# Kernel tuning notes

Hardware: AMD Instinct MI355X
Metric: run time of the kernel (lower is better)

Reference implementation:

```python
import jax, jax.numpy as jnp
import numpy as np

B, F, H, LAT = 4, 64, 128, 512
N_CALLS = 16          # n_calls=2, module multiplies by 8
NEG = 0.2             # leaky-relu slope
EPS = 1e-5            # InstanceNorm2d eps

# hypernetwork output layout: w_in[F,3F], b_in[F], w_mid[F,F], b_mid[F], w_out[F,F], b_out[F], w_short[F,3F], b_short[F]
_sizes = [3*F*F, F, F*F, F, F*F, F, 3*F*F, F]
_off = np.cumsum([0] + _sizes)
HYP_OUT = int(_off[-1])


def _sobel_kernel():
    # SinSobel: smoothing (cos) x derivative (sin) separable 5x5 gradient filters
    lin = np.linspace(-1.0, 1.0, 5)
    d = np.sin(lin * np.pi / 2.0)
    s = np.cos(lin * np.pi / 2.0)
    gx = np.outer(s, d)                      # d/dx
    gy = np.outer(d, s)                      # d/dy
    k = np.stack([gx, gy])[:, None]          # [2,1,5,5]
    return jnp.asarray(np.tile(k, (F, 1, 1, 1)), jnp.float32)  # [2F,1,5,5] depthwise


def _conv(x, w, pad, groups=1):
    return jax.lax.conv_general_dilated(
        x, w, (1, 1), [(pad, pad), (pad, pad)],
        dimension_numbers=('NCHW', 'OIHW', 'NCHW'),
        feature_group_count=groups)


def _lrelu(x):
    return jnp.where(x >= 0, x, NEG * x)


def setup_inputs() -> dict:
    key = jax.random.key(0)
    ks = jax.random.split(key, 8)
    f32 = jnp.float32
    return {
        "lat": jax.random.normal(ks[0], (B, LAT), f32),
        "ca_init": jax.random.normal(ks[1], (B, F, H, H), f32),
        "leak_factor": jnp.asarray(0.1, f32),
        "hyper_w": jax.random.normal(ks[2], (HYP_OUT, LAT), f32) * 0.02,
        "hyper_b": jnp.zeros((HYP_OUT,), f32),
        "res_w1": jax.random.normal(ks[3], (F, F, 3, 3), f32) * 0.05,
        "res_b1": jnp.zeros((F,), f32),
        "res_w2": jax.random.normal(ks[4], (F, F, 3, 3), f32) * 0.05,
        "res_b2": jnp.zeros((F,), f32),
        "img_w": jax.random.normal(ks[5], (3, F, 3, 3), f32) * 0.05,
        "img_b": jnp.zeros((3,), f32),
    }


def reference(lat, ca_init, leak_factor, hyper_w, hyper_b,
              res_w1, res_b1, res_w2, res_b2, img_w, img_b):
    sob = _sobel_kernel()
    lf = jnp.clip(leak_factor, 0.001, 1000.0)

    # per-sample dynamic 1x1-conv weights from hypernetwork (lat is loop-invariant)
    ws = lat @ hyper_w.T + hyper_b           # [B, HYP_OUT]

    def seg(i, shape):
        return ws[:, _off[i]:_off[i + 1]].reshape((B,) + shape)
    w_in,  b_in  = seg(0, (F, 3 * F)), seg(1, (F,))
    w_mid, b_mid = seg(2, (F, F)),     seg(3, (F,))
    w_out, b_out = seg(4, (F, F)),     seg(5, (F,))
    w_sh,  b_sh  = seg(6, (F, 3 * F)), seg(7, (F,))

    def step(out, _):
        # SinSobel: identity channels + depthwise 5x5 gradients -> [B,3F,H,H]
        y = jnp.concatenate([out, _conv(out, sob, 2, groups=F)], axis=1)
        # InstanceNorm2d (affine=False)
        mu = y.mean((2, 3), keepdims=True)
        var = y.var((2, 3), keepdims=True)
        y = (y - mu) * jax.lax.rsqrt(var + EPS)
        # DynaResidualBlock: per-sample 1x1 convs (batched GEMMs) + shortcut
        h = _lrelu(jnp.einsum('bchw,boc->bohw', y, w_in) + b_in[:, :, None, None])
        h = _lrelu(jnp.einsum('bchw,boc->bohw', h, w_mid) + b_mid[:, :, None, None])
        h = jnp.einsum('bchw,boc->bohw', h, w_out) + b_out[:, :, None, None]
        sc = jnp.einsum('bchw,boc->bohw', y, w_sh) + b_sh[:, :, None, None]
        return out + lf * (h + sc), None

    out, _ = jax.lax.scan(step, ca_init, None, length=N_CALLS)

    # conv_img: ResidualBlock(3x3) then final 3x3 conv to image channels, clamp
    h = _lrelu(_conv(out, res_w1, 1) + res_b1[None, :, None, None])
    h = _conv(h, res_w2, 1) + res_b2[None, :, None, None]
    out = out + h
    img = _conv(out, img_w, 1) + img_b[None, :, None, None]
    return jnp.clip(img, -1.0, 1.0)
```

## Files before the change

### kernel.cpp

```cpp
#include <hip/hip_runtime.h>
#include <cstddef>

#define R_ 0.70710678118654752f
#define NEG_ 0.2f
#define EPS_ 1e-5f

constexpr int F_ = 64, C3_ = 192, HH_ = 128, NPIX_ = 16384, B_ = 4, LAT_ = 512, HYP_ = 33024;
constexpr int OFFI_WIN = 0, OFFI_BIN = 12288, OFFI_WMID = 12352, OFFI_BMID = 16448,
              OFFI_WOUT = 16512, OFFI_BOUT = 20608, OFFI_WSH = 20672, OFFI_BSH = 32960;
constexpr size_t OFF_HYP = 0;
constexpr size_t OFF_SRAW = 134144;
constexpr size_t OFF_WFIN = 140288;
constexpr size_t OFF_WFSH = 189440;
constexpr size_t OFF_WFMID = 238592;
constexpr size_t OFF_WFOUT = 254976;
constexpr size_t OFF_CW1 = 271360;
constexpr size_t OFF_CW2 = 308224;
constexpr size_t OFF_CWIMG = 345088;
constexpr size_t OFF_OUT = 346816;
constexpr size_t OFF_SOB = 4541120;
constexpr size_t OFF_TMP = OFF_SOB;

typedef short bf16x8 __attribute__((ext_vector_type(8)));
typedef float f32x4 __attribute__((ext_vector_type(4)));

static __device__ __forceinline__ unsigned short f2b(float v) {
  unsigned u = __builtin_bit_cast(unsigned, v);
  u += 0x7fffu + ((u >> 16) & 1u);
  return (unsigned short)(u >> 16);
}
static __device__ __forceinline__ float b2f(unsigned short h) {
  return __builtin_bit_cast(float, ((unsigned)h) << 16);
}
static __device__ __forceinline__ void split2(float v, unsigned short& hi, unsigned short& lo) {
  hi = f2b(v);
  lo = f2b(v - b2f(hi));
}

#define MM3(acc, ahi, alo, whi, wlo)                                        \
  acc = __builtin_amdgcn_mfma_f32_16x16x32_bf16(ahi, whi, acc, 0, 0, 0);    \
  acc = __builtin_amdgcn_mfma_f32_16x16x32_bf16(ahi, wlo, acc, 0, 0, 0);    \
  acc = __builtin_amdgcn_mfma_f32_16x16x32_bf16(alo, whi, acc, 0, 0, 0);

__global__ __launch_bounds__(256) void hyper_gemm_kernel(
    const float* __restrict__ lat, const float* __restrict__ hw,
    const float* __restrict__ hb, float* __restrict__ hyp) {
  __shared__ float slat[B_ * LAT_];
  const int tid = threadIdx.x;
  for (int i = tid; i < B_ * LAT_; i += 256) slat[i] = lat[i];
  __syncthreads();
  const int wave = tid >> 6, lane = tid & 63;
  const int j = blockIdx.x * 4 + wave;
  if (j >= HYP_) return;
  const float* wr = hw + (size_t)j * LAT_;
  float a0 = 0.f, a1 = 0.f, a2 = 0.f, a3 = 0.f;
  for (int i = 0; i < LAT_; i += 64) {
    float w = wr[i + lane];
    a0 = __builtin_fmaf(w, slat[0 * LAT_ + i + lane], a0);
    a1 = __builtin_fmaf(w, slat[1 * LAT_ + i + lane], a1);
    a2 = __builtin_fmaf(w, slat[2 * LAT_ + i + lane], a2);
    a3 = __builtin_fmaf(w, slat[3 * LAT_ + i + lane], a3);
  }
  #pragma unroll
  for (int off = 32; off; off >>= 1) {
    a0 += __shfl_down(a0, off, 64);
    a1 += __shfl_down(a1, off, 64);
    a2 += __shfl_down(a2, off, 64);
    a3 += __shfl_down(a3, off, 64);
  }
  if (lane == 0) {
    float b = hb[j];
    hyp[0 * HYP_ + j] = a0 + b;
    hyp[1 * HYP_ + j] = a1 + b;
    hyp[2 * HYP_ + j] = a2 + b;
    hyp[3 * HYP_ + j] = a3 + b;
  }
}

__global__ __launch_bounds__(256) void prep_dynw_kernel(float* wsm) {
  const int b = blockIdx.x >> 3, sl = blockIdx.x & 7;
  const int tid = threadIdx.x;
  const float* hyp = wsm + OFF_HYP + (size_t)b * HYP_;
  unsigned short* wfin = (unsigned short*)(wsm + OFF_WFIN) + (size_t)b * 24576;
  unsigned short* wfsh = (unsigned short*)(wsm + OFF_WFSH) + (size_t)b * 24576;
  unsigned short* wfmid = (unsigned short*)(wsm + OFF_WFMID) + (size_t)b * 8192;
  unsigned short* wfout = (unsigned short*)(wsm + OFF_WFOUT) + (size_t)b * 8192;

  if (sl < 6) {
    const int base = sl * 2048;
    for (int i = tid; i < 2048; i += 256) {
      int idx = base + i;
      int j = idx & 7, ch = (idx >> 3) & 63, g2 = (idx >> 9) & 3, ks = idx >> 11;
      int k = ks * 32 + g2 * 8 + j;
      int fbx = ((ks * 4 + g2) * 64 + ch) * 16;
      unsigned short h, l;
      split2(hyp[OFFI_WIN + ch * C3_ + k], h, l);
      wfin[fbx + j] = h; wfin[fbx + 8 + j] = l;
      split2(hyp[OFFI_WSH + ch * C3_ + k], h, l);
      wfsh[fbx + j] = h; wfsh[fbx + 8 + j] = l;
    }
  } else if (sl == 6) {
    for (int idx = tid; idx < 4096; idx += 256) {
      int j = idx & 7, ch = (idx >> 3) & 63, g2 = (idx >> 9) & 3, ks = idx >> 11;
      int k = ks * 32 + g2 * 8 + j;
      int fbx = ((ks * 4 + g2) * 64 + ch) * 16;
      unsigned short h, l;
      split2(hyp[OFFI_WMID + ch * 64 + k], h, l);
      wfmid[fbx + j] = h; wfmid[fbx + 8 + j] = l;
      split2(hyp[OFFI_WOUT + ch * 64 + k], h, l);
      wfout[fbx + j] = h; wfout[fbx + 8 + j] = l;
    }
  }
}

__global__ __launch_bounds__(256) void prep_convw_kernel(
    const float* __restrict__ w1, const float* __restrict__ w2,
    const float* __restrict__ wi, unsigned short* __restrict__ wf1,
    unsigned short* __restrict__ wf2, float* __restrict__ wit) {
  const int idx = blockIdx.x * 256 + threadIdx.x;
  if (idx < 36864) {
    int j = idx & 7, ch = (idx >> 3) & 63, fg = idx >> 9;
    int k = (fg >> 2) * 32 + (fg & 3) * 8 + j;
    int c = k & 63, t = k >> 6;
    int fb = (fg * 64 + ch) * 16;
    unsigned short h, l;
    split2(w1[(ch * 64 + c) * 9 + t], h, l);
    wf1[fb + j] = h; wf1[fb + 8 + j] = l;
    split2(w2[(ch * 64 + c) * 9 + t], h, l);
    wf2[fb + j] = h; wf2[fb + 8 + j] = l;
  }
  if (idx < 64 * 9 * 3) {
    int k = idx % 3, rest = idx / 3;
    int t = rest % 9, c = rest / 9;
    wit[idx] = wi[(k * 64 + c) * 9 + t];
  }
}

__device__ __forceinline__ float blockReduceSum(float v, float* scratch) {
  const int tid = threadIdx.x;
  #pragma unroll
  for (int off = 32; off; off >>= 1) v += __shfl_down(v, off, 64);
  if ((tid & 63) == 0) scratch[tid >> 6] = v;
  __syncthreads();
  float r = scratch[0] + scratch[1] + scratch[2] + scratch[3];
  __syncthreads();
  return r;
}

__device__ __forceinline__ void hline_z(const float* __restrict__ P, int rr, int col,
                                        float& hdv, float& hsv, float& cv) {
  if (rr < 0 || rr > 127) { hdv = 0.f; hsv = 0.f; cv = 0.f; return; }
  const float* rp = P + rr * HH_;
  float vm2 = (col >= 2) ? rp[col - 2] : 0.f;
  float vm1 = (col >= 1) ? rp[col - 1] : 0.f;
  float v0 = rp[col];
  float vp1 = (col <= 126) ? rp[col + 1] : 0.f;
  float vp2 = (col <= 125) ? rp[col + 2] : 0.f;
  hdv = -vm2 - R_ * vm1 + R_ * vp1 + vp2;
  hsv = R_ * vm1 + v0 + R_ * vp1;
  cv = v0;
}

__global__ __launch_bounds__(256) void sobel_stats_kernel(
    const float* __restrict__ outb, unsigned int* __restrict__ sob,
    float* __restrict__ sraw) {
  __shared__ float scr[4];
  const int bi = blockIdx.x;
  const int q = bi & 3, c = (bi >> 2) & 63, b = bi >> 8;
  const int tid = threadIdx.x;
  const int col = tid & 127;
  const int r0 = q * 32 + (tid >> 7) * 16;
  const float* P = outb + ((size_t)(b * F_ + c)) * NPIX_;
  unsigned int* ygx = sob + ((size_t)(b * 128 + 2 * c)) * NPIX_;
  unsigned int* ygy = ygx + NPIX_;

  float sI = 0.f, qI = 0.f, sX = 0.f, qX = 0.f, sY = 0.f, qY = 0.f;
  float hd_m1, hd_0, hd_p1, hs_m2, hs_m1, hs_0, hs_p1;
  float td, tc;
  hline_z(P, r0 - 2, col, td, hs_m2, tc);
  hline_z(P, r0 - 1, col, hd_m1, hs_m1, tc);
  hline_z(P, r0, col, hd_0, hs_0, tc);
  sI += tc; qI += tc * tc;
  hline_z(P, r0 + 1, col, hd_p1, hs_p1, tc);
  sI += tc; qI += tc * tc;

  for (int i = 0; i < 16; ++i) {
    const int r = r0 + i;
    const int nr = r + 2;
    float hd_new, hs_new, cnew;
    hline_z(P, nr, col, hd_new, hs_new, cnew);
    if (nr <= r0 + 15) { sI += cnew; qI += cnew * cnew; }
    float gxv = R_ * (hd_m1 + hd_p1) + hd_0;
    float gyv = -hs_m2 - R_ * hs_m1 + R_ * hs_p1 + hs_new;
    const int o = r * HH_ + col;
    unsigned short h, l;
    split2(gxv, h, l);
    ygx[o] = ((unsigned)h << 16) | l;
    split2(gyv, h, l);
    ygy[o] = ((unsigned)h << 16) | l;
    sX += gxv; qX += gxv * gxv;
    sY += gyv; qY += gyv * gyv;
    hd_m1 = hd_0; hd_0 = hd_p1; hd_p1 = hd_new;
    hs_m2 = hs_m1; hs_m1 = hs_0; hs_0 = hs_p1; hs_p1 = hs_new;
  }
  __syncthreads();
  float tI = blockReduceSum(sI, scr);
  float tQI = blockReduceSum(qI, scr);
  float tX = blockReduceSum(sX, scr);
  float tQX = blockReduceSum(qX, scr);
  float tY = blockReduceSum(sY, scr);
  float tQY = blockReduceSum(qY, scr);
  if (tid == 0) {
    float* r = sraw + (size_t)bi * 6;
    r[0] = tI; r[1] = tQI; r[2] = tX; r[3] = tQX; r[4] = tY; r[5] = tQY;
  }
}

__global__ __launch_bounds__(256, 2) void mlp_mfma_kernel(
    float* __restrict__ outb, const unsigned int* __restrict__ sobu,
    const float* __restrict__ wsf, const float* __restrict__ leak) {
  __shared__ unsigned short yhi[64 * 200];
  __shared__ unsigned short ylo[64 * 200];
  __shared__ unsigned short hhi[64 * 72];
  __shared__ unsigned short hlo[64 * 72];
  __shared__ unsigned short resb[64 * 66];
  __shared__ float stl[C3_ * 2];
  __shared__ float ssig[64];
  const int bi = blockIdx.x;
  const int b = bi >> 8, t = bi & 255;
  const int px0 = t * 64;
  const int tid = threadIdx.x;

  if (tid < 64) {
    const int c = tid;
    const float* r = wsf + OFF_SRAW + ((size_t)(b * 64 + c) * 4) * 6;
    float sI = 0.f, qI = 0.f, sX = 0.f, qX = 0.f, sY = 0.f, qY = 0.f;
    #pragma unroll
    for (int q = 0; q < 4; ++q) {
      sI += r[q * 6 + 0]; qI += r[q * 6 + 1];
      sX += r[q * 6 + 2]; qX += r[q * 6 + 3];
      sY += r[q * 6 + 4]; qY += r[q * 6 + 5];
    }
    const float n = 1.f / 16384.f;
    float m, rs;
    m = sI * n; rs = rsqrtf(qI * n - m * m + EPS_);
    stl[c * 2] = m; stl[c * 2 + 1] = rs; ssig[c] = 1.f / rs;
    const int cx = 64 + 2 * c, cy = cx + 1;
    m = sX * n; stl[cx * 2] = m;          stl[cx * 2 + 1] = rsqrtf(qX * n - m * m + EPS_);
    m = sY * n; stl[cy * 2] = m;          stl[cy * 2 + 1] = rsqrtf(qY * n - m * m + EPS_);
  }
  __syncthreads();

  const float* ob = outb + (size_t)b * F_ * NPIX_;
  const unsigned int* sbp = sobu + (size_t)b * 128 * NPIX_;
  #pragma unroll
  for (int it = 0; it < 12; ++it) {
    int ci = it * 256 + tid;
    int k = ci >> 4, pq = ci & 15;
    int kk = k ^ ((pq >> 1) << 3);
    unsigned short* ph = &yhi[(pq * 4) * 200 + kk];
    unsigned short* pl = &ylo[(pq * 4) * 200 + kk];
    const float mu = stl[k * 2], inv = stl[k * 2 + 1];
    float vv[4];
    if (k < 64) {
      float4 f = *(const float4*)(ob + (size_t)k * NPIX_ + px0 + pq * 4);
      vv[0] = f.x; vv[1] = f.y; vv[2] = f.z; vv[3] = f.w;
      const float sg = ssig[k];
      #pragma unroll
      for (int e = 0; e < 4; ++e) {
        unsigned short h, l;
        split2((vv[e] - mu) * inv, h, l);
        ph[e * 200] = h; pl[e * 200] = l;
        float rec = __builtin_fmaf(b2f(h) + b2f(l), sg, mu);
        resb[k * 66 + pq * 4 + e] = f2b(vv[e] - rec);
      }
    } else {
      uint4 v = *(const uint4*)(sbp + (size_t)(k - 64) * NPIX_ + px0 + pq * 4);
      vv[0] = b2f((unsigned short)(v.x >> 16)) + b2f((unsigned short)(v.x & 0xffff));
      vv[1] = b2f((unsigned short)(v.y >> 16)) + b2f((unsigned short)(v.y & 0xffff));
      vv[2] = b2f((unsigned short)(v.z >> 16)) + b2f((unsigned short)(v.z & 0xffff));
      vv[3] = b2f((unsigned short)(v.w >> 16)) + b2f((unsigned short)(v.w & 0xffff));
      #pragma unroll
      for (int e = 0; e < 4; ++e) {
        unsigned short h, l;
        split2((vv[e] - mu) * inv, h, l);
        ph[e * 200] = h; pl[e * 200] = l;
      }
    }
  }
  __syncthreads();

  const int wave = tid >> 6, lane = tid & 63;
  const int lrow = lane & 15, g = lane >> 4;
  const int chm = wave * 16 + lrow;
  const float lf = fminf(fmaxf(leak[0], 0.001f), 1000.f);
  const float* hyp = wsf + OFF_HYP + (size_t)b * HYP_;
  const unsigned short* wfin = (const unsigned short*)(wsf + OFF_WFIN) + (size_t)b * 24576;
  const unsigned short* wfsh = (const unsigned short*)(wsf + OFF_WFSH) + (size_t)b * 24576;
  const unsigned short* wfmid = (const unsigned short*)(wsf + OFF_WFMID) + (size_t)b * 8192;
  const unsigned short* wfout = (const unsigned short*)(wsf + OFF_WFOUT) + (size_t)b * 8192;

  f32x4 aH[4], aS[4];
  {
    float b1 = hyp[OFFI_BIN + chm], b2 = hyp[OFFI_BSH + chm];
    #pragma unroll
    for (int pf = 0; pf < 4; ++pf) {
      aH[pf] = (f32x4){b1, b1, b1, b1};
      aS[pf] = (f32x4){b2, b2, b2, b2};
    }
  }
  #pragma unroll
  for (int ks = 0; ks < 6; ++ks) {
    const size_t wo = (size_t)((ks * 4 + g) * 64 + chm) * 16;
    bf16x8 whiI = *(const bf16x8*)(wfin + wo);
    bf16x8 wloI = *(const bf16x8*)(wfin + wo + 8);
    bf16x8 whiS = *(const bf16x8*)(wfsh + wo);
    bf16x8 wloS = *(const bf16x8*)(wfsh + wo + 8);
    #pragma unroll
    for (int pf = 0; pf < 4; ++pf) {
      const int pxl = pf * 16 + lrow;
      const int kb = pxl * 200 + ((ks * 32 + g * 8) ^ ((pxl >> 3) << 3));
      bf16x8 ahi = *(const bf16x8*)&yhi[kb];
      bf16x8 alo = *(const bf16x8*)&ylo[kb];
      MM3(aH[pf], ahi, alo, whiI, wloI);
      MM3(aS[pf], ahi, alo, whiS, wloS);
    }
  }
  #pragma unroll
  for (int pf = 0; pf < 4; ++pf) {
    #pragma unroll
    for (int j = 0; j < 4; ++j) {
      float v = aH[pf][j];
      v = (v >= 0.f) ? v : NEG_ * v;
      unsigned short h, l;
      split2(v, h, l);
      const int o = (pf * 16 + g * 4 + j) * 72 + chm;
      hhi[o] = h; hlo[o] = l;
    }
  }
  __syncthreads();
  f32x4 aM[4];
  {
    float bm = hyp[OFFI_BMID + chm];
    #pragma unroll
    for (int pf = 0; pf < 4; ++pf) aM[pf] = (f32x4){bm, bm, bm, bm};
  }
  #pragma unroll
  for (int ks = 0; ks < 2; ++ks) {
    const size_t wo = (size_t)((ks * 4 + g) * 64 + chm) * 16;
    bf16x8 whi = *(const bf16x8*)(wfmid + wo);
    bf16x8 wlo = *(const bf16x8*)(wfmid + wo + 8);
    #pragma unroll
    for (int pf = 0; pf < 4; ++pf) {
      const int kb = (pf * 16 + lrow) * 72 + ks * 32 + g * 8;
      bf16x8 ahi = *(const bf16x8*)&hhi[kb];
      bf16x8 alo = *(const bf16x8*)&hlo[kb];
      MM3(aM[pf], ahi, alo, whi, wlo);
    }
  }
  __syncthreads();
  #pragma unroll
  for (int pf = 0; pf < 4; ++pf) {
    #pragma unroll
    for (int j = 0; j < 4; ++j) {
      float v = aM[pf][j];
      v = (v >= 0.f) ? v : NEG_ * v;
      unsigned short h, l;
      split2(v, h, l);
      const int o = (pf * 16 + g * 4 + j) * 72 + chm;
      hhi[o] = h; hlo[o] = l;
    }
  }
  __syncthreads();
  f32x4 aO[4];
  {
    float bo = hyp[OFFI_BOUT + chm];
    #pragma unroll
    for (int pf = 0; pf < 4; ++pf) aO[pf] = (f32x4){bo, bo, bo, bo};
  }
  #pragma unroll
  for (int ks = 0; ks < 2; ++ks) {
    const size_t wo = (size_t)((ks * 4 + g) * 64 + chm) * 16;
    bf16x8 whi = *(const bf16x8*)(wfout + wo);
    bf16x8 wlo = *(const bf16x8*)(wfout + wo + 8);
    #pragma unroll
    for (int pf = 0; pf < 4; ++pf) {
      const int kb = (pf * 16 + lrow) * 72 + ks * 32 + g * 8;
      bf16x8 ahi = *(const bf16x8*)&hhi[kb];
      bf16x8 alo = *(const bf16x8*)&hlo[kb];
      MM3(aO[pf], ahi, alo, whi, wlo);
    }
  }
  const float mu_c = stl[chm * 2];
  const float sg_c = ssig[chm];
  #pragma unroll
  for (int pf = 0; pf < 4; ++pf) {
    float* op = outb + ((size_t)(b * F_ + chm)) * NPIX_ + px0 + pf * 16 + g * 4;
    f32x4 nv;
    #pragma unroll
    for (int j = 0; j < 4; ++j) {
      const int pxl = pf * 16 + g * 4 + j;
      const int kk2 = chm ^ ((pxl >> 3) << 3);
      float yv = b2f(yhi[pxl * 200 + kk2]) + b2f(ylo[pxl * 200 + kk2]);
      float vorig = __builtin_fmaf(yv, sg_c, mu_c) + b2f(resb[chm * 66 + pxl]);
      nv[j] = vorig + lf * (aO[pf][j] + aS[pf][j]);
    }
    *(f32x4*)op = nv;
  }
}

__global__ __launch_bounds__(256, 2) void conv_mfma_kernel(
    const float* __restrict__ in, const unsigned short* __restrict__ wf,
    const float* __restrict__ bias, float* __restrict__ dst, int mode) {
  __shared__ unsigned short ahi[3 * 72 * 64];
  __shared__ unsigned short alo[3 * 72 * 64];
  const int bi = blockIdx.x;
  const int b = bi >> 8, tile = bi & 255;
  const int row = tile >> 1, colbase = (tile & 1) << 6;
  const int tid = threadIdx.x;
  const float* ip = in + (size_t)b * F_ * NPIX_;

  for (int idx = tid; idx < 3456; idx += 256) {
    const int chunk = idx % 18;
    const int rowp = (idx / 18) % 3;
    const int ch = idx / 54;
    const int r2 = row - 1 + rowp;
    const int gcol0 = colbase - 4 + chunk * 4;
    float4 v;
    if (r2 < 0 || r2 > 127) {
      v = make_float4(0.f, 0.f, 0.f, 0.f);
    } else if (gcol0 >= 0 && gcol0 <= 124) {
      v = *(const float4*)(ip + (size_t)ch * NPIX_ + r2 * HH_ + gcol0);
    } else {
      const float* rp = ip + (size_t)ch * NPIX_ + r2 * HH_;
      v.x = (gcol0 >= 0 && gcol0 < 128) ? rp[gcol0] : 0.f;
      v.y = (gcol0 + 1 >= 0 && gcol0 + 1 < 128) ? rp[gcol0 + 1] : 0.f;
      v.z = (gcol0 + 2 >= 0 && gcol0 + 2 < 128) ? rp[gcol0 + 2] : 0.f;
      v.w = (gcol0 + 3 >= 0 && gcol0 + 3 < 128) ? rp[gcol0 + 3] : 0.f;
    }
    const float vv[4] = {v.x, v.y, v.z, v.w};
    #pragma unroll
    for (int e = 0; e < 4; ++e) {
      const int i = chunk * 4 + e;
      const int sw = (((i >> 2) & 7) ^ ((i & 3) << 1) ^ rowp) << 3;
      const int a = (rowp * 72 + i) * 64 + (ch ^ sw);
      unsigned short h, l;
      split2(vv[e], h, l);
      ahi[a] = h; alo[a] = l;
    }
  }
  __syncthreads();

  const int wave = tid >> 6, lane = tid & 63;
  const int lrow = lane & 15, g = lane >> 4;
  const int pxl = wave * 16 + lrow;
  f32x4 acc[4];
  #pragma unroll
  for (int cg = 0; cg < 4; ++cg) {
    float bz = bias[cg * 16 + lrow];
    acc[cg] = (f32x4){bz, bz, bz, bz};
  }
  for (int ks = 0; ks < 18; ++ks) {
    const int kbase = ks * 32 + g * 8;
    const int t = kbase >> 6, c0 = kbase & 63;
    const int dy = t / 3 - 1, dx = t % 3 - 1;
    const int rowp = 1 + dy;
    const int i = pxl + 4 + dx;
    const int sw = (((i >> 2) & 7) ^ ((i & 3) << 1) ^ rowp) << 3;
    const int a = (rowp * 72 + i) * 64 + (c0 ^ sw);
    bf16x8 a_hi = *(const bf16x8*)&ahi[a];
    bf16x8 a_lo = *(const bf16x8*)&alo[a];
    #pragma unroll
    for (int cg = 0; cg < 4; ++cg) {
      const unsigned short* wp = wf + (size_t)((ks * 4 + g) * 64 + cg * 16 + lrow) * 16;
      bf16x8 whi = *(const bf16x8*)wp;
      bf16x8 wlo = *(const bf16x8*)(wp + 8);
      MM3(acc[cg], a_hi, a_lo, whi, wlo);
    }
  }
  #pragma unroll
  for (int cg = 0; cg < 4; ++cg) {
    float* op = dst + ((size_t)(b * F_ + cg * 16 + lrow)) * NPIX_ + row * HH_ + colbase +
                wave * 16 + g * 4;
    if (mode == 1) {
      f32x4 r;
      #pragma unroll
      for (int j = 0; j < 4; ++j) {
        float v = acc[cg][j];
        r[j] = (v >= 0.f) ? v : NEG_ * v;
      }
      *(f32x4*)op = r;
    } else {
      f32x4 cur = *(f32x4*)op;
      #pragma unroll
      for (int j = 0; j < 4; ++j) cur[j] += acc[cg][j];
      *(f32x4*)op = cur;
    }
  }
}

__global__ __launch_bounds__(256, 4) void convimg_kernel(
    const float* __restrict__ outb, const float* __restrict__ wT,
    const float* __restrict__ bias, float* __restrict__ img) {
  __shared__ float part[2 * 128 * 3];
  const int bi = blockIdx.x;
  const int b = bi >> 7, pxb = bi & 127;
  const int tid = threadIdx.x;
  const int px = tid & 127;
  const int hf = __builtin_amdgcn_readfirstlane(tid >> 7);
  const int p = pxb * 128 + px;
  const int row = p >> 7, col = p & 127;
  float a0 = 0.f, a1 = 0.f, a2 = 0.f;
  const float* ip = outb + (size_t)b * F_ * NPIX_;
  for (int cc = 0; cc < 32; ++cc) {
    const int c = hf * 32 + cc;
    const float* pl = ip + (size_t)c * NPIX_;
    #pragma unroll
    for (int t = 0; t < 9; ++t) {
      const int dy = t / 3 - 1, dx = t % 3 - 1;
      const int r2 = row + dy, c2 = col + dx;
      float v = (r2 >= 0 && r2 < 128 && c2 >= 0 && c2 < 128) ? pl[r2 * HH_ + c2] : 0.f;
      const float* wp = wT + (c * 9 + t) * 3;
      a0 = __builtin_fmaf(v, wp[0], a0);
      a1 = __builtin_fmaf(v, wp[1], a1);
      a2 = __builtin_fmaf(v, wp[2], a2);
    }
  }
  part[(hf * 128 + px) * 3 + 0] = a0;
  part[(hf * 128 + px) * 3 + 1] = a1;
  part[(hf * 128 + px) * 3 + 2] = a2;
  __syncthreads();
  if (hf == 0) {
    float r0 = a0 + part[(128 + px) * 3 + 0] + bias[0];
    float r1 = a1 + part[(128 + px) * 3 + 1] + bias[1];
    float r2 = a2 + part[(128 + px) * 3 + 2] + bias[2];
    img[((size_t)b * 3 + 0) * NPIX_ + p] = fminf(fmaxf(r0, -1.f), 1.f);
    img[((size_t)b * 3 + 1) * NPIX_ + p] = fminf(fmaxf(r1, -1.f), 1.f);
    img[((size_t)b * 3 + 2) * NPIX_ + p] = fminf(fmaxf(r2, -1.f), 1.f);
  }
}

extern "C" void kernel_launch(void* const* d_in, const int* in_sizes, int n_in,
                              void* d_out, int out_size, void* d_ws, size_t ws_size,
                              hipStream_t stream) {
  const float* lat = (const float*)d_in[0];
  const float* ca_init = (const float*)d_in[1];
  const float* leak = (const float*)d_in[2];
  const float* hyper_w = (const float*)d_in[3];
  const float* hyper_b = (const float*)d_in[4];
  const float* res_w1 = (const float*)d_in[5];
  const float* res_b1 = (const float*)d_in[6];
  const float* res_w2 = (const float*)d_in[7];
  const float* res_b2 = (const float*)d_in[8];
  const float* img_w = (const float*)d_in[9];
  const float* img_b = (const float*)d_in[10];
  float* out = (float*)d_out;
  float* ws = (float*)d_ws;
  unsigned int* sobu = (unsigned int*)(ws + OFF_SOB);

  hyper_gemm_kernel<<<(HYP_ + 3) / 4, 256, 0, stream>>>(lat, hyper_w, hyper_b, ws + OFF_HYP);
  prep_dynw_kernel<<<32, 256, 0, stream>>>(ws);
  prep_convw_kernel<<<144, 256, 0, stream>>>(res_w1, res_w2, img_w,
                                             (unsigned short*)(ws + OFF_CW1),
                                             (unsigned short*)(ws + OFF_CW2),
                                             ws + OFF_CWIMG);
  hipMemcpyAsync(ws + OFF_OUT, ca_init, (size_t)B_ * F_ * NPIX_ * sizeof(float),
                 hipMemcpyDeviceToDevice, stream);

  for (int st = 0; st < 16; ++st) {
    sobel_stats_kernel<<<1024, 256, 0, stream>>>(ws + OFF_OUT, sobu, ws + OFF_SRAW);
    mlp_mfma_kernel<<<1024, 256, 0, stream>>>(ws + OFF_OUT, sobu, ws, leak);
  }

  conv_mfma_kernel<<<1024, 256, 0, stream>>>(ws + OFF_OUT, (const unsigned short*)(ws + OFF_CW1),
                                             res_b1, (float*)(ws + OFF_TMP), 1);
  conv_mfma_kernel<<<1024, 256, 0, stream>>>((const float*)(ws + OFF_TMP),
                                             (const unsigned short*)(ws + OFF_CW2),
                                             res_b2, ws + OFF_OUT, 2);
  convimg_kernel<<<512, 256, 0, stream>>>(ws + OFF_OUT, ws + OFF_CWIMG, img_b, out);
}
```

Before: 944.0 us.

## Prefetch MLP tile loads before stats sync; compute two rows per conv block

In the MLP kernel, the 12 global loads of state and Sobel data are now issued into registers before the per-channel statistics reduction and barrier. This lets their latency overlap with that work. The 3x3 conv kernel now computes two output rows per block, staging four input rows in shared memory so each weight fragment loaded from global memory feeds two MFMA chains. This halves the conv grid and increases register and shared-memory use per block.

New measurement: 945.5 us. Within noise of the previous version (+0.2%).

```diff
diff --git a/kernel.cpp b/kernel.cpp
--- a/kernel.cpp
+++ b/kernel.cpp
@@ -231,6 +231,19 @@
   const int px0 = t * 64;
   const int tid = threadIdx.x;
 
+  const float* ob = outb + (size_t)b * F_ * NPIX_;
+  const unsigned int* sbp = sobu + (size_t)b * 128 * NPIX_;
+  uint4 vbuf[12];
+  #pragma unroll
+  for (int it = 0; it < 12; ++it) {
+    const int ci = it * 256 + tid;
+    const int k = ci >> 4, pq = ci & 15;
+    const unsigned int* src =
+        (k < 64) ? (const unsigned int*)(ob + (size_t)k * NPIX_ + px0 + pq * 4)
+                 : (sbp + (size_t)(k - 64) * NPIX_ + px0 + pq * 4);
+    vbuf[it] = *(const uint4*)src;
+  }
+
   if (tid < 64) {
     const int c = tid;
     const float* r = wsf + OFF_SRAW + ((size_t)(b * 64 + c) * 4) * 6;
@@ -251,21 +264,19 @@
   }
   __syncthreads();
 
-  const float* ob = outb + (size_t)b * F_ * NPIX_;
-  const unsigned int* sbp = sobu + (size_t)b * 128 * NPIX_;
   #pragma unroll
   for (int it = 0; it < 12; ++it) {
-    int ci = it * 256 + tid;
-    int k = ci >> 4, pq = ci & 15;
-    int kk = k ^ ((pq >> 1) << 3);
+    const int ci = it * 256 + tid;
+    const int k = ci >> 4, pq = ci & 15;
+    const int kk = k ^ ((pq >> 1) << 3);
     unsigned short* ph = &yhi[(pq * 4) * 200 + kk];
     unsigned short* pl = &ylo[(pq * 4) * 200 + kk];
     const float mu = stl[k * 2], inv = stl[k * 2 + 1];
-    float vv[4];
+    const uint4 v = vbuf[it];
     if (k < 64) {
-      float4 f = *(const float4*)(ob + (size_t)k * NPIX_ + px0 + pq * 4);
-      vv[0] = f.x; vv[1] = f.y; vv[2] = f.z; vv[3] = f.w;
       const float sg = ssig[k];
+      const float vv[4] = {__builtin_bit_cast(float, v.x), __builtin_bit_cast(float, v.y),
+                           __builtin_bit_cast(float, v.z), __builtin_bit_cast(float, v.w)};
       #pragma unroll
       for (int e = 0; e < 4; ++e) {
         unsigned short h, l;
@@ -275,15 +286,12 @@
         resb[k * 66 + pq * 4 + e] = f2b(vv[e] - rec);
       }
     } else {
-      uint4 v = *(const uint4*)(sbp + (size_t)(k - 64) * NPIX_ + px0 + pq * 4);
-      vv[0] = b2f((unsigned short)(v.x >> 16)) + b2f((unsigned short)(v.x & 0xffff));
-      vv[1] = b2f((unsigned short)(v.y >> 16)) + b2f((unsigned short)(v.y & 0xffff));
-      vv[2] = b2f((unsigned short)(v.z >> 16)) + b2f((unsigned short)(v.z & 0xffff));
-      vv[3] = b2f((unsigned short)(v.w >> 16)) + b2f((unsigned short)(v.w & 0xffff));
+      const unsigned uu[4] = {v.x, v.y, v.z, v.w};
       #pragma unroll
       for (int e = 0; e < 4; ++e) {
+        float val = b2f((unsigned short)(uu[e] >> 16)) + b2f((unsigned short)(uu[e] & 0xffff));
         unsigned short h, l;
-        split2((vv[e] - mu) * inv, h, l);
+        split2((val - mu) * inv, h, l);
         ph[e * 200] = h; pl[e * 200] = l;
       }
     }
@@ -412,19 +420,19 @@
 __global__ __launch_bounds__(256, 2) void conv_mfma_kernel(
     const float* __restrict__ in, const unsigned short* __restrict__ wf,
     const float* __restrict__ bias, float* __restrict__ dst, int mode) {
-  __shared__ unsigned short ahi[3 * 72 * 64];
-  __shared__ unsigned short alo[3 * 72 * 64];
+  __shared__ unsigned short ahi[4 * 72 * 64];
+  __shared__ unsigned short alo[4 * 72 * 64];
   const int bi = blockIdx.x;
-  const int b = bi >> 8, tile = bi & 255;
-  const int row = tile >> 1, colbase = (tile & 1) << 6;
+  const int b = bi >> 7, rest = bi & 127;
+  const int row0 = (rest >> 1) * 2, colbase = (rest & 1) << 6;
   const int tid = threadIdx.x;
   const float* ip = in + (size_t)b * F_ * NPIX_;
 
-  for (int idx = tid; idx < 3456; idx += 256) {
+  for (int idx = tid; idx < 4608; idx += 256) {
     const int chunk = idx % 18;
-    const int rowp = (idx / 18) % 3;
-    const int ch = idx / 54;
-    const int r2 = row - 1 + rowp;
+    const int rowp = (idx / 18) % 4;
+    const int ch = idx / 72;
+    const int r2 = row0 - 1 + rowp;
     const int gcol0 = colbase - 4 + chunk * 4;
     float4 v;
     if (r2 < 0 || r2 > 127) {
@@ -454,47 +462,57 @@
   const int wave = tid >> 6, lane = tid & 63;
   const int lrow = lane & 15, g = lane >> 4;
   const int pxl = wave * 16 + lrow;
-  f32x4 acc[4];
+  f32x4 acc0[4], acc1[4];
   #pragma unroll
   for (int cg = 0; cg < 4; ++cg) {
     float bz = bias[cg * 16 + lrow];
-    acc[cg] = (f32x4){bz, bz, bz, bz};
+    acc0[cg] = (f32x4){bz, bz, bz, bz};
+    acc1[cg] = (f32x4){bz, bz, bz, bz};
   }
   for (int ks = 0; ks < 18; ++ks) {
     const int kbase = ks * 32 + g * 8;
     const int t = kbase >> 6, c0 = kbase & 63;
     const int dy = t / 3 - 1, dx = t % 3 - 1;
-    const int rowp = 1 + dy;
     const int i = pxl + 4 + dx;
-    const int sw = (((i >> 2) & 7) ^ ((i & 3) << 1) ^ rowp) << 3;
-    const int a = (rowp * 72 + i) * 64 + (c0 ^ sw);
-    bf16x8 a_hi = *(const bf16x8*)&ahi[a];
-    bf16x8 a_lo = *(const bf16x8*)&alo[a];
+    const int rp0 = 1 + dy, rp1 = 2 + dy;
+    const int sw0 = (((i >> 2) & 7) ^ ((i & 3) << 1) ^ rp0) << 3;
+    const int sw1 = (((i >> 2) & 7) ^ ((i & 3) << 1) ^ rp1) << 3;
+    const int a0 = (rp0 * 72 + i) * 64 + (c0 ^ sw0);
+    const int a1 = (rp1 * 72 + i) * 64 + (c0 ^ sw1);
+    bf16x8 ah0 = *(const bf16x8*)&ahi[a0];
+    bf16x8 al0 = *(const bf16x8*)&alo[a0];
+    bf16x8 ah1 = *(const bf16x8*)&ahi[a1];
+    bf16x8 al1 = *(const bf16x8*)&alo[a1];
     #pragma unroll
     for (int cg = 0; cg < 4; ++cg) {
       const unsigned short* wp = wf + (size_t)((ks * 4 + g) * 64 + cg * 16 + lrow) * 16;
       bf16x8 whi = *(const bf16x8*)wp;
       bf16x8 wlo = *(const bf16x8*)(wp + 8);
-      MM3(acc[cg], a_hi, a_lo, whi, wlo);
-    }
-  }
-  #pragma unroll
-  for (int cg = 0; cg < 4; ++cg) {
-    float* op = dst + ((size_t)(b * F_ + cg * 16 + lrow)) * NPIX_ + row * HH_ + colbase +
-                wave * 16 + g * 4;
-    if (mode == 1) {
-      f32x4 r;
-      #pragma unroll
-      for (int j = 0; j < 4; ++j) {
-        float v = acc[cg][j];
-        r[j] = (v >= 0.f) ? v : NEG_ * v;
+      MM3(acc0[cg], ah0, al0, whi, wlo);
+      MM3(acc1[cg], ah1, al1, whi, wlo);
+    }
+  }
+  #pragma unroll
+  for (int r = 0; r < 2; ++r) {
+    #pragma unroll
+    for (int cg = 0; cg < 4; ++cg) {
+      const f32x4 av = r ? acc1[cg] : acc0[cg];
+      float* op = dst + ((size_t)(b * F_ + cg * 16 + lrow)) * NPIX_ + (row0 + r) * HH_ +
+                  colbase + wave * 16 + g * 4;
+      if (mode == 1) {
+        f32x4 rr;
+        #pragma unroll
+        for (int j = 0; j < 4; ++j) {
+          float v = av[j];
+          rr[j] = (v >= 0.f) ? v : NEG_ * v;
+        }
+        *(f32x4*)op = rr;
+      } else {
+        f32x4 cur = *(f32x4*)op;
+        #pragma unroll
+        for (int j = 0; j < 4; ++j) cur[j] += av[j];
+        *(f32x4*)op = cur;
       }
-      *(f32x4*)op = r;
-    } else {
-      f32x4 cur = *(f32x4*)op;
-      #pragma unroll
-      for (int j = 0; j < 4; ++j) cur[j] += acc[cg][j];
-      *(f32x4*)op = cur;
     }
   }
 }
@@ -572,10 +590,10 @@
     mlp_mfma_kernel<<<1024, 256, 0, stream>>>(ws + OFF_OUT, sobu, ws, leak);
   }
 
-  conv_mfma_kernel<<<1024, 256, 0, stream>>>(ws + OFF_OUT, (const unsigned short*)(ws + OFF_CW1),
-                                             res_b1, (float*)(ws + OFF_TMP), 1);
-  conv_mfma_kernel<<<1024, 256, 0, stream>>>((const float*)(ws + OFF_TMP),
-                                             (const unsigned short*)(ws + OFF_CW2),
-                                             res_b2, ws + OFF_OUT, 2);
+  conv_mfma_kernel<<<512, 256, 0, stream>>>(ws + OFF_OUT, (const unsigned short*)(ws + OFF_CW1),
+                                            res_b1, (float*)(ws + OFF_TMP), 1);
+  conv_mfma_kernel<<<512, 256, 0, stream>>>((const float*)(ws + OFF_TMP),
+                                            (const unsigned short*)(ws + OFF_CW2),
+                                            res_b2, ws + OFF_OUT, 2);
   convimg_kernel<<<512, 256, 0, stream>>>(ws + OFF_OUT, ws + OFF_CWIMG, img_b, out);
 }
```
